# Kernel optimization log

Measured on AMD Instinct MI355X. Metric: run time of the kernel, lower is better.

Reference implementation:

```python
import jax, jax.numpy as jnp
import numpy as np

H1 = 51  # lstm1 hidden size
H3 = 1   # lstm3 hidden size


def _lstm_cell(x, h, c, W_ih, W_hh, b_ih, b_hh):
    # PyTorch LSTMCell: gates ordered (i, f, g, o)
    g = x @ W_ih.T + b_ih + h @ W_hh.T + b_hh
    i, f, gg, o = jnp.split(g, 4, axis=-1)
    c2 = jax.nn.sigmoid(f) * c + jax.nn.sigmoid(i) * jnp.tanh(gg)
    h2 = jax.nn.sigmoid(o) * jnp.tanh(c2)
    return h2, c2


def setup_inputs() -> dict:
    key = jax.random.key(0)
    ks = jax.random.split(key, 9)
    B, T = 2048, 2000
    s1 = 1.0 / np.sqrt(H1)
    s3 = 1.0 / np.sqrt(H3)
    u = lambda k, shape, s: jax.random.uniform(k, shape, jnp.float32, -s, s)
    return {
        "input": jax.random.normal(ks[0], (B, T), jnp.float32),
        "W_ih1": u(ks[1], (4 * H1, 1), s1),
        "W_hh1": u(ks[2], (4 * H1, H1), s1),
        "b_ih1": u(ks[3], (4 * H1,), s1),
        "b_hh1": u(ks[4], (4 * H1,), s1),
        "W_ih3": u(ks[5], (4 * H3, H1), s3),
        "W_hh3": u(ks[6], (4 * H3, H3), s3),
        "b_ih3": u(ks[7], (4 * H3,), s3),
        "b_hh3": u(ks[8], (4 * H3,), s3),
        "future": 0,
    }


def reference(input, W_ih1, W_hh1, b_ih1, b_hh1, W_ih3, W_hh3, b_ih3, b_hh3, future):
    B, T = input.shape
    dt = input.dtype
    h1 = jnp.zeros((B, H1), dt)
    c1 = jnp.zeros((B, H1), dt)
    h3 = jnp.zeros((B, H3), dt)
    c3 = jnp.zeros((B, H3), dt)

    def step(carry, x_t):
        h1, c1, h3, c3 = carry
        h1, c1 = _lstm_cell(x_t, h1, c1, W_ih1, W_hh1, b_ih1, b_hh1)
        # NOTE: original feeds c_t (cell state) into lstm3 and emits c_t3
        h3, c3 = _lstm_cell(c1, h3, c3, W_ih3, W_hh3, b_ih3, b_hh3)
        return (h1, c1, h3, c3), c3

    xs = input.T[:, :, None]  # [T, B, 1]
    carry, outs = jax.lax.scan(step, (h1, c1, h3, c3), xs)

    if future > 0:
        def fstep(carry, _):
            h1, c1, h3, c3 = carry
            h1, c1 = _lstm_cell(c3, h1, c1, W_ih1, W_hh1, b_ih1, b_hh1)
            h3, c3 = _lstm_cell(c1, h3, c3, W_ih3, W_hh3, b_ih3, b_hh3)
            return (h1, c1, h3, c3), c3

        carry, fouts = jax.lax.scan(fstep, carry, None, length=future)
        outs = jnp.concatenate([outs, fouts], axis=0)

    # [T(+future), B, 1] -> [B, T(+future)]
    return outs[:, :, 0].T
```

## Files before the change

kernel.cpp:

```cpp
#include <hip/hip_runtime.h>
#include <hip/hip_bf16.h>

#define SEQT 2000
#define NB   2048
#define H1   51
#define MROW 16
#define NBLK (NB / MROW)
#define PADK 168
#define OSTR 65

#define L2E  1.4426950408889634f
#define L2E2 2.8853900817779268f

typedef float f32x4 __attribute__((ext_vector_type(4)));
typedef short s16x8 __attribute__((ext_vector_type(8)));
typedef unsigned u32x4 __attribute__((ext_vector_type(4)));
typedef unsigned u32x2 __attribute__((ext_vector_type(2)));

#if __has_builtin(__builtin_amdgcn_exp2f)
#define EXP2F(x) __builtin_amdgcn_exp2f(x)
#else
#define EXP2F(x) __expf((x) * 0.6931471805599453f)
#endif

template <bool B> struct BoolC { static constexpr bool value = B; };

__device__ __forceinline__ short f2bf(float f) { __hip_bfloat16 b(f); return *(short*)&b; }
__device__ __forceinline__ float bf2f(short s) { __hip_bfloat16 b; *(short*)&b = s; return (float)b; }
__device__ __forceinline__ float rbf(float f) { return bf2f(f2bf(f)); }
__device__ __forceinline__ float fastrcp(float x) { return __builtin_amdgcn_rcpf(x); }
__device__ __forceinline__ float tanhfast(float x) {
    return 1.f - 2.f * fastrcp(EXP2F(x * L2E2) + 1.f);
}

__device__ __forceinline__ unsigned rne_bf16(float v) {
    unsigned b = __float_as_uint(v);
    return (b + 0x7fffu + ((b >> 16) & 1u)) >> 16;
}
__device__ __forceinline__ unsigned pack_hilo(float v) {
    const unsigned hh = rne_bf16(v);
    const float hi = __uint_as_float(hh << 16);
    const unsigned hl = rne_bf16(v - hi);
    return hh | (hl << 16);
}

__device__ __forceinline__ f32x4 mfma16(s16x8 a, s16x8 b, f32x4 c) {
    return __builtin_amdgcn_mfma_f32_16x16x32_bf16(a, b, c, 0, 0, 0);
}


__device__ __forceinline__ float aval(const float* __restrict__ W_hh1,
                                      const float* __restrict__ W_ih1,
                                      const float* __restrict__ b_ih1,
                                      const float* __restrict__ b_hh1,
                                      int n, float sc, bool vr, int k) {
    if (!vr) return 0.f;
    if (k < 96) {
        const int gp = k >> 3, j = k & 7;
        const int u = 4 * ((gp >> 2) * 4 + (j >> 1)) + (gp & 3);
        return rbf(sc * W_hh1[n * H1 + u]);
    } else if (k < 102) {
        const int u = 48 + ((k - 96) >> 1);
        return rbf(sc * W_hh1[n * H1 + u]);
    } else if (k < 104) {
        return rbf(sc * W_ih1[n]);
    } else if (k < 152) {
        const int d = k - 104;
        const int gp = d >> 2;
        const int u = 4 * ((gp >> 2) * 4 + (d & 3)) + (gp & 3);
        const float wv = sc * W_hh1[n * H1 + u];
        return wv - rbf(wv);
    } else if (k < 155) {
        const int u = 48 + (k - 152);
        const float wv = sc * W_hh1[n * H1 + u];
        return wv - rbf(wv);
    } else if (k == 155) {
        const float wv = sc * W_ih1[n];
        return wv - rbf(wv);
    } else if (k == 156) {
        return rbf(sc * (b_ih1[n] + b_hh1[n]));
    } else if (k == 157) {
        const float bv = sc * (b_ih1[n] + b_hh1[n]);
        return bv - rbf(bv);
    }
    return 0.f;
}

template <int SL, int NTc>
__device__ __forceinline__ void run_tiles(const s16x8 (&Wfr)[4][5], const s16x8 (&hf)[5],
                                          float (&c1st)[4], short* __restrict__ Hw,
                                          float* __restrict__ C1w,
                                          const int iloc, const int kq) {
    f32x4 acc[4];
#pragma unroll
    for (int i = 0; i < NTc; ++i) {
        f32x4 a = (f32x4){0.f, 0.f, 0.f, 0.f};
        a = mfma16(Wfr[i][0], hf[0], a);
        a = mfma16(Wfr[i][1], hf[1], a);
        a = mfma16(Wfr[i][2], hf[2], a);
        a = mfma16(Wfr[i][3], hf[3], a);
        a = mfma16(Wfr[i][4], hf[4], a);
        acc[i] = a;
    }
    unsigned hp[4];
    float cl[4];
#pragma unroll
    for (int i = 0; i < NTc; ++i) {
        const float ei = EXP2F(acc[i][0]);
        const float ef = EXP2F(acc[i][1]);
        const float eg = EXP2F(acc[i][2]);
        const float eo = EXP2F(acc[i][3]);
        const float pf = 1.f + ef, pi_ = 1.f + ei, pg = 1.f + eg, mg = 1.f - eg;
        const float pp = pi_ * pg;
        float c1 = c1st[i];
        c1 = fmaf(c1, pp, pf * mg) * fastrcp(pf * pp);
        c1st[i] = c1;
        cl[i] = c1;
        const float ec = EXP2F(fminf(115.4f, c1 * -L2E2));
        const float h1 = (1.f - ec) * fastrcp((1.f + eo) * (1.f + ec));
        const __hip_bfloat16 bh(h1);
        const float df = h1 - (float)bh;
        const __hip_bfloat16 bl(df);
        hp[i] = (unsigned)*(const unsigned short*)&bh |
                ((unsigned)*(const unsigned short*)&bl << 16);
    }
    const int base = iloc * PADK;
    if (NTc == 4) {
        *(u32x4*)&Hw[base + (SL * 4 + kq) * 8] =
            (u32x4){hp[0], hp[1], hp[2], hp[3]};
        const unsigned s01 = (hp[0] & 0xffffu) | (hp[1] << 16);
        const unsigned s23 = (hp[2] & 0xffffu) | (hp[3] << 16);
        *(u32x2*)&Hw[base + 104 + (SL * 4 + kq) * 4] = (u32x2){s01, s23};
        *(f32x4*)&C1w[iloc * 52 + SL * 16 + kq * 4] =
            (f32x4){cl[0], cl[1], cl[2], cl[3]};
    } else {
        const bool ok = (48 + kq) < H1;
        *(unsigned*)&Hw[base + (ok ? 96 + 2 * kq : 160)] = hp[0];
        Hw[base + (ok ? 152 + kq : 164)] = (short)hp[0];
        C1w[iloc * 52 + 48 + kq] = cl[0];
    }
}

__device__ __forceinline__ void xchunk_fill(const float* __restrict__ input, int r0, int c,
                                            int lane, unsigned (*Xb)[64 * 16]) {
    const int m = lane & 15, q = lane >> 4;
    const int tt = c * 64 + q * 16;
    f32x4 v[4];
    if (tt < SEQT) {
        const float* src = input + (size_t)(r0 + m) * SEQT + tt;
#pragma unroll
        for (int p = 0; p < 4; ++p) v[p] = *(const f32x4*)(src + 4 * p);
    } else {
#pragma unroll
        for (int p = 0; p < 4; ++p) v[p] = (f32x4){0.f, 0.f, 0.f, 0.f};
    }
#pragma unroll
    for (int p = 0; p < 4; ++p)
#pragma unroll
        for (int j = 0; j < 4; ++j)
            Xb[c & 1][(q * 16 + p * 4 + j) * 16 + m] = pack_hilo(v[p][j]);
}

__global__ void __launch_bounds__(256)
__attribute__((amdgpu_waves_per_eu(1)))
lstm_fused_kernel(const float* __restrict__ input,
                  const float* __restrict__ W_ih1,
                  const float* __restrict__ W_hh1,
                  const float* __restrict__ b_ih1,
                  const float* __restrict__ b_hh1,
                  const float* __restrict__ W_ih3,
                  const float* __restrict__ W_hh3,
                  const float* __restrict__ b_ih3,
                  const float* __restrict__ b_hh3,
                  float* __restrict__ out) {
    const int t = threadIdx.x;
    const int w = t >> 6;
    const int lane = t & 63;
    const int iloc = lane & 15, kq = lane >> 4;
    const int r0 = blockIdx.x * MROW;

    __shared__ short Hst[2][MROW * PADK];
    __shared__ float C1buf[2][MROW * 52];
    __shared__ float Obuf[2][MROW * OSTR];
    __shared__ unsigned Xbuf[2][64 * 16];

    const int NT = (w == 1) ? 1 : 4;
    const int tb = (w == 0) ? 0 : (w == 1) ? 12 : (w == 2) ? 4 : 8;

    s16x8 Wfr[4][5];
#pragma unroll
    for (int i = 0; i < 4; ++i) {
        if (i < NT) {
            const int np = (tb + i) * 16 + iloc;
            const int u_r = np >> 2, g_r = np & 3;
            const int n = g_r * H1 + u_r;
            const bool vr = (u_r < H1);
            const float sc = (g_r == 2) ? -L2E2 : -L2E;
#pragma unroll
            for (int kt = 0; kt < 5; ++kt) {
                s16x8 bf;
#pragma unroll
                for (int j = 0; j < 8; ++j)
                    bf[j] = f2bf(aval(W_hh1, W_ih1, b_ih1, b_hh1, n, sc, vr,
                                      kt * 32 + kq * 8 + j));
                Wfr[i][kt] = bf;
            }
        }
    }

    const int g3 = lane >> 4;
    const float scg3 = (g3 == 2) ? L2E2 : -L2E;
    float Wz[52];
    if (w == 1) {
#pragma unroll
        for (int p = 0; p < 52; ++p) {
            const int u = (p < 48) ? (16 * (p >> 4) + 4 * (p & 3) + ((p >> 2) & 3))
                                   : p;
            Wz[p] = (u < H1) ? scg3 * W_ih3[g3 * H1 + u] : 0.f;
        }
    }
    const float whh3g = scg3 * W_hh3[g3];
    const float b3g = scg3 * (b_ih3[g3] + b_hh3[g3]);
    const float ag = (g3 == 2) ? -2.f : 1.f;
    const float bg = (g3 == 2) ? 1.f : 0.f;

    for (int idx = t; idx < 2 * MROW * PADK; idx += 256)
        ((short*)Hst)[idx] = 0;
    for (int idx = t; idx < 2 * MROW * 52; idx += 256)
        ((float*)C1buf)[idx] = 0.f;
    __syncthreads();
    if (t < MROW) {
        const int m = t;
#pragma unroll
        for (int p = 0; p < 2; ++p) {
            Hst[p][m * PADK + 156] = (short)0x3F80;
            Hst[p][m * PADK + 157] = (short)0x3F80;
        }
        const float x0 = input[(size_t)(r0 + m) * SEQT];
        const unsigned xp = pack_hilo(x0);
        Hst[1][m * PADK + 102] = (short)xp;
        Hst[1][m * PADK + 103] = (short)(xp >> 16);
        Hst[1][m * PADK + 155] = (short)xp;
    }
    if (w == 1) {
        xchunk_fill(input, r0, 0, lane, Xbuf);
        xchunk_fill(input, r0, 1, lane, Xbuf);
    }
    float c1st[4] = {0.f, 0.f, 0.f, 0.f};
    float h3 = 0.f, c3 = 0.f;
    float h3b = 0.f;

    auto lstm3_step = [&](const f32x4 (&c1v)[13], int s) {
        float d0a = 0.f, d1a = 0.f, d2a = 0.f, d3a = 0.f;
        float d0b = 0.f, d1b = 0.f, d2b = 0.f, d3b = 0.f;
#pragma unroll
        for (int j = 0; j < 13; ++j) {
            if ((j & 1) == 0) {
                d0a = fmaf(Wz[4 * j + 0], c1v[j][0], d0a);
                d1a = fmaf(Wz[4 * j + 1], c1v[j][1], d1a);
                d2a = fmaf(Wz[4 * j + 2], c1v[j][2], d2a);
                d3a = fmaf(Wz[4 * j + 3], c1v[j][3], d3a);
            } else {
                d0b = fmaf(Wz[4 * j + 0], c1v[j][0], d0b);
                d1b = fmaf(Wz[4 * j + 1], c1v[j][1], d1b);
                d2b = fmaf(Wz[4 * j + 2], c1v[j][2], d2b);
                d3b = fmaf(Wz[4 * j + 3], c1v[j][3], d3b);
            }
        }
        const float z = ((d0a + d0b) + (d1a + d1b)) +
                        ((d2a + d2b) + (d3a + d3b));
        const float pre = z + fmaf(whh3g, h3b, b3g);
        const float act = bg + ag * fastrcp(EXP2F(pre) + 1.f);
        const float act1 = __shfl_xor(act, 16, 64);
        const float act2 = __shfl_xor(act, 32, 64);
        const float act3 = __shfl_xor(act, 48, 64);
        if (lane < MROW) {
            c3 = act1 * c3 + act * act2;
            h3 = act3 * tanhfast(c3);
            Obuf[(s >> 6) & 1][lane * OSTR + (s & 63)] = c3;
        }
        h3b = __shfl(h3, lane & 15, 64);
    };

    auto do_pair = [&](const int tsE, auto fillc, auto dumpc) {
        constexpr bool FILL = decltype(fillc)::value;
        constexpr bool DUMP = decltype(dumpc)::value;
        unsigned pv2 = 0;
        __syncthreads();
        {
            s16x8 hf[5];
#pragma unroll
            for (int kt = 0; kt < 5; ++kt)
                hf[kt] = *(const s16x8*)&Hst[1][iloc * PADK + kt * 32 + kq * 8];
            f32x4 c1v[13];
            unsigned pv1 = 0;
            if (w == 1) {
                const float* cr = &C1buf[1][(lane & 15) * 52];
#pragma unroll
                for (int j = 0; j < 13; ++j)
                    c1v[j] = *(const f32x4*)(cr + 4 * j);
                const int t1 = tsE + 1;
                pv1 = Xbuf[(t1 >> 6) & 1][(t1 & 63) * 16 + (lane & 15)];
                if (tsE + 2 < SEQT) {
                    const int t2 = tsE + 2;
                    pv2 = Xbuf[(t2 >> 6) & 1][(t2 & 63) * 16 + (lane & 15)];
                }
            }
            f32x4 xv[4];
            if (FILL && w == 1) {
                const int fc = (tsE >> 6) + 1;
                const int fm = lane & 15, fq = lane >> 4;
                const int tt = fc * 64 + fq * 16;
                if (tt < SEQT) {
                    const float* src = input + (size_t)(r0 + fm) * SEQT + tt;
#pragma unroll
                    for (int p = 0; p < 4; ++p) xv[p] = *(const f32x4*)(src + 4 * p);
                } else {
#pragma unroll
                    for (int p = 0; p < 4; ++p) xv[p] = (f32x4){0.f, 0.f, 0.f, 0.f};
                }
            }
            short* Hw = &Hst[0][0];
            float* C1w = &C1buf[0][0];
            if (w == 0) {
                run_tiles<0, 4>(Wfr, hf, c1st, Hw, C1w, iloc, kq);
            } else if (w == 2) {
                run_tiles<1, 4>(Wfr, hf, c1st, Hw, C1w, iloc, kq);
            } else if (w == 3) {
                run_tiles<2, 4>(Wfr, hf, c1st, Hw, C1w, iloc, kq);
            } else {
                const int m2 = lane & 15;
                *(unsigned*)&Hw[m2 * PADK + 102] = pv1;
                Hw[m2 * PADK + 155] = (short)pv1;
                run_tiles<3, 1>(Wfr, hf, c1st, Hw, C1w, iloc, kq);
                if (tsE > 0)
                    lstm3_step(c1v, tsE - 1);
            }
            if (FILL && w == 1) {
                const int fc = (tsE >> 6) + 1;
                const int fm = lane & 15, fq = lane >> 4;
#pragma unroll
                for (int p = 0; p < 4; ++p)
#pragma unroll
                    for (int j = 0; j < 4; ++j)
                        Xbuf[fc & 1][(fq * 16 + p * 4 + j) * 16 + fm] =
                            pack_hilo(xv[p][j]);
            }
        }
        __syncthreads();
        {
            const int tsO = tsE + 1;
            s16x8 hf[5];
#pragma unroll
            for (int kt = 0; kt < 5; ++kt)
                hf[kt] = *(const s16x8*)&Hst[0][iloc * PADK + kt * 32 + kq * 8];
            f32x4 c1v[13];
            if (w == 1) {
                const float* cr = &C1buf[0][(lane & 15) * 52];
#pragma unroll
                for (int j = 0; j < 13; ++j)
                    c1v[j] = *(const f32x4*)(cr + 4 * j);
            }
            if (DUMP) {
                const int c = (tsO >> 6) - 1;
#pragma unroll
                for (int rep = 0; rep < 4; ++rep) {
                    const int row = w + 4 * rep;
                    out[(size_t)(r0 + row) * SEQT + c * 64 + lane] =
                        Obuf[c & 1][row * OSTR + lane];
                }
            }
            short* Hw = &Hst[1][0];
            float* C1w = &C1buf[1][0];
            if (w == 0) {
                run_tiles<0, 4>(Wfr, hf, c1st, Hw, C1w, iloc, kq);
            } else if (w == 2) {
                run_tiles<1, 4>(Wfr, hf, c1st, Hw, C1w, iloc, kq);
            } else if (w == 3) {
                run_tiles<2, 4>(Wfr, hf, c1st, Hw, C1w, iloc, kq);
            } else {
                if (tsE + 2 < SEQT) {
                    const int m2 = lane & 15;
                    *(unsigned*)&Hw[m2 * PADK + 102] = pv2;
                    Hw[m2 * PADK + 155] = (short)pv2;
                }
                run_tiles<3, 1>(Wfr, hf, c1st, Hw, C1w, iloc, kq);
                lstm3_step(c1v, tsO - 1);
            }
        }
    };

#pragma unroll 1
    for (int c = 0; c < 32; ++c) {
        const int base = c << 6;
        int p0 = 0;
        if (c >= 1 && c < 31) {
            do_pair(base, BoolC<true>{}, BoolC<true>{});
            p0 = 1;
        } else if (c == 31) {
            do_pair(base, BoolC<false>{}, BoolC<true>{});
            p0 = 1;
        }
        const int npairs = (c == 31) ? 8 : 32;
#pragma unroll 1
        for (int p = p0; p < npairs; ++p)
            do_pair(base + (p << 1), BoolC<false>{}, BoolC<false>{});
    }

    __syncthreads();
    if (w == 1) {
        f32x4 c1v[13];
        const float* cr = &C1buf[1][(lane & 15) * 52];
#pragma unroll
        for (int j = 0; j < 13; ++j)
            c1v[j] = *(const f32x4*)(cr + 4 * j);
        lstm3_step(c1v, SEQT - 1);
    }

    __syncthreads();
    {
        const int row = t >> 4, pos = t & 15;
        out[(size_t)(r0 + row) * SEQT + 1984 + pos] = Obuf[1][row * OSTR + pos];
    }
}

extern "C" void kernel_launch(void* const* d_in, const int* in_sizes, int n_in,
                              void* d_out, int out_size, void* d_ws, size_t ws_size,
                              hipStream_t stream) {
    const float* input = (const float*)d_in[0];
    const float* W_ih1 = (const float*)d_in[1];
    const float* W_hh1 = (const float*)d_in[2];
    const float* b_ih1 = (const float*)d_in[3];
    const float* b_hh1 = (const float*)d_in[4];
    const float* W_ih3 = (const float*)d_in[5];
    const float* W_hh3 = (const float*)d_in[6];
    const float* b_ih3 = (const float*)d_in[7];
    const float* b_hh3 = (const float*)d_in[8];
    float* out = (float*)d_out;

    lstm_fused_kernel<<<NBLK, 256, 0, stream>>>(
        input, W_ih1, W_hh1, b_ih1, b_hh1, W_ih3, W_hh3, b_ih3, b_hh3, out);
}
```

Measured before the change: 1.298 ms.

## Distribute lstm3 input projection across waves and specialize per-wave loops

Each wave now folds its own c1 values into partial lstm3 gate dot-products (4 gates) right after computing them, and writes 16 partial sums per row to shared memory. This replaces the 52-element c1 buffer and the serial 52-term dot product on wave 1. The pair loop is also templated on wave id, first and last step, so branches become compile-time and each wave gets its own specialized code path. The cost moves into more FMAs per wave and a larger unrolled code body, in exchange for a shorter critical path on wave 1.

```diff
diff --git a/kernel.cpp b/kernel.cpp
--- a/kernel.cpp
+++ b/kernel.cpp
@@ -24,6 +24,7 @@
 #endif
 
 template <bool B> struct BoolC { static constexpr bool value = B; };
+template <int V>  struct IntC  { static constexpr int  value = V; };
 
 __device__ __forceinline__ short f2bf(float f) { __hip_bfloat16 b(f); return *(short*)&b; }
 __device__ __forceinline__ float bf2f(short s) { __hip_bfloat16 b; *(short*)&b = s; return (float)b; }
@@ -88,8 +89,9 @@
 
 template <int SL, int NTc>
 __device__ __forceinline__ void run_tiles(const s16x8 (&Wfr)[4][5], const s16x8 (&hf)[5],
-                                          float (&c1st)[4], short* __restrict__ Hw,
-                                          float* __restrict__ C1w,
+                                          float (&c1st)[4], const float (&W3c)[4][4],
+                                          short* __restrict__ Hw,
+                                          float* __restrict__ Zw,
                                           const int iloc, const int kq) {
     f32x4 acc[4];
 #pragma unroll
@@ -103,7 +105,7 @@
         acc[i] = a;
     }
     unsigned hp[4];
-    float cl[4];
+    float zp0 = 0.f, zp1 = 0.f, zp2 = 0.f, zp3 = 0.f;
 #pragma unroll
     for (int i = 0; i < NTc; ++i) {
         const float ei = EXP2F(acc[i][0]);
@@ -115,7 +117,10 @@
         float c1 = c1st[i];
         c1 = fmaf(c1, pp, pf * mg) * fastrcp(pf * pp);
         c1st[i] = c1;
-        cl[i] = c1;
+        zp0 = fmaf(W3c[i][0], c1, zp0);
+        zp1 = fmaf(W3c[i][1], c1, zp1);
+        zp2 = fmaf(W3c[i][2], c1, zp2);
+        zp3 = fmaf(W3c[i][3], c1, zp3);
         const float ec = EXP2F(fminf(115.4f, c1 * -L2E2));
         const float h1 = (1.f - ec) * fastrcp((1.f + eo) * (1.f + ec));
         const __hip_bfloat16 bh(h1);
@@ -131,14 +136,12 @@
         const unsigned s01 = (hp[0] & 0xffffu) | (hp[1] << 16);
         const unsigned s23 = (hp[2] & 0xffffu) | (hp[3] << 16);
         *(u32x2*)&Hw[base + 104 + (SL * 4 + kq) * 4] = (u32x2){s01, s23};
-        *(f32x4*)&C1w[iloc * 52 + SL * 16 + kq * 4] =
-            (f32x4){cl[0], cl[1], cl[2], cl[3]};
     } else {
         const bool ok = (48 + kq) < H1;
         *(unsigned*)&Hw[base + (ok ? 96 + 2 * kq : 160)] = hp[0];
         Hw[base + (ok ? 152 + kq : 164)] = (short)hp[0];
-        C1w[iloc * 52 + 48 + kq] = cl[0];
-    }
+    }
+    *(f32x4*)Zw = (f32x4){zp0, zp1, zp2, zp3};
 }
 
 __device__ __forceinline__ void xchunk_fill(const float* __restrict__ input, int r0, int c,
@@ -180,9 +183,9 @@
     const int r0 = blockIdx.x * MROW;
 
     __shared__ short Hst[2][MROW * PADK];
-    __shared__ float C1buf[2][MROW * 52];
     __shared__ float Obuf[2][MROW * OSTR];
     __shared__ unsigned Xbuf[2][64 * 16];
+    __shared__ float Zbuf[2][16][16][4];
 
     const int NT = (w == 1) ? 1 : 4;
     const int tb = (w == 0) ? 0 : (w == 1) ? 12 : (w == 2) ? 4 : 8;
@@ -208,17 +211,18 @@
         }
     }
 
+    float W3c[4][4];
+#pragma unroll
+    for (int i = 0; i < 4; ++i) {
+        const int u = (tb + i) * 4 + kq;
+        const bool ok = (i < NT) && (u < H1);
+#pragma unroll
+        for (int g = 0; g < 4; ++g)
+            W3c[i][g] = ok ? ((g == 2) ? L2E2 : -L2E) * W_ih3[g * H1 + u] : 0.f;
+    }
+
     const int g3 = lane >> 4;
     const float scg3 = (g3 == 2) ? L2E2 : -L2E;
-    float Wz[52];
-    if (w == 1) {
-#pragma unroll
-        for (int p = 0; p < 52; ++p) {
-            const int u = (p < 48) ? (16 * (p >> 4) + 4 * (p & 3) + ((p >> 2) & 3))
-                                   : p;
-            Wz[p] = (u < H1) ? scg3 * W_ih3[g3 * H1 + u] : 0.f;
-        }
-    }
     const float whh3g = scg3 * W_hh3[g3];
     const float b3g = scg3 * (b_ih3[g3] + b_hh3[g3]);
     const float ag = (g3 == 2) ? -2.f : 1.f;
@@ -226,8 +230,6 @@
 
     for (int idx = t; idx < 2 * MROW * PADK; idx += 256)
         ((short*)Hst)[idx] = 0;
-    for (int idx = t; idx < 2 * MROW * 52; idx += 256)
-        ((float*)C1buf)[idx] = 0.f;
     __syncthreads();
     if (t < MROW) {
         const int m = t;
@@ -250,25 +252,12 @@
     float h3 = 0.f, c3 = 0.f;
     float h3b = 0.f;
 
-    auto lstm3_step = [&](const f32x4 (&c1v)[13], int s) {
-        float d0a = 0.f, d1a = 0.f, d2a = 0.f, d3a = 0.f;
-        float d0b = 0.f, d1b = 0.f, d2b = 0.f, d3b = 0.f;
-#pragma unroll
-        for (int j = 0; j < 13; ++j) {
-            if ((j & 1) == 0) {
-                d0a = fmaf(Wz[4 * j + 0], c1v[j][0], d0a);
-                d1a = fmaf(Wz[4 * j + 1], c1v[j][1], d1a);
-                d2a = fmaf(Wz[4 * j + 2], c1v[j][2], d2a);
-                d3a = fmaf(Wz[4 * j + 3], c1v[j][3], d3a);
-            } else {
-                d0b = fmaf(Wz[4 * j + 0], c1v[j][0], d0b);
-                d1b = fmaf(Wz[4 * j + 1], c1v[j][1], d1b);
-                d2b = fmaf(Wz[4 * j + 2], c1v[j][2], d2b);
-                d3b = fmaf(Wz[4 * j + 3], c1v[j][3], d3b);
-            }
-        }
-        const float z = ((d0a + d0b) + (d1a + d1b)) +
-                        ((d2a + d2b) + (d3a + d3b));
+    auto lstm3_step = [&](const float (&zv)[16], int s) {
+        const float z =
+            (((zv[0] + zv[1]) + (zv[2] + zv[3])) +
+             ((zv[4] + zv[5]) + (zv[6] + zv[7]))) +
+            (((zv[8] + zv[9]) + (zv[10] + zv[11])) +
+             ((zv[12] + zv[13]) + (zv[14] + zv[15])));
         const float pre = z + fmaf(whh3g, h3b, b3g);
         const float act = bg + ag * fastrcp(EXP2F(pre) + 1.f);
         const float act1 = __shfl_xor(act, 16, 64);
@@ -282,9 +271,14 @@
         h3b = __shfl(h3, lane & 15, 64);
     };
 
-    auto do_pair = [&](const int tsE, auto fillc, auto dumpc) {
-        constexpr bool FILL = decltype(fillc)::value;
-        constexpr bool DUMP = decltype(dumpc)::value;
+    auto do_pair = [&](auto wc, auto fc, auto dc, auto fic, auto lac,
+                       const int tsE) {
+        constexpr int W = decltype(wc)::value;
+        constexpr bool FILL = decltype(fc)::value;
+        constexpr bool DUMP = decltype(dc)::value;
+        constexpr bool FIRST = decltype(fic)::value;
+        constexpr bool LAST = decltype(lac)::value;
+        constexpr int SL = (W == 0) ? 0 : (W == 1) ? 3 : (W == 2) ? 1 : 2;
         unsigned pv2 = 0;
         __syncthreads();
         {
@@ -292,25 +286,26 @@
 #pragma unroll
             for (int kt = 0; kt < 5; ++kt)
                 hf[kt] = *(const s16x8*)&Hst[1][iloc * PADK + kt * 32 + kq * 8];
-            f32x4 c1v[13];
+            float zv[16];
             unsigned pv1 = 0;
-            if (w == 1) {
-                const float* cr = &C1buf[1][(lane & 15) * 52];
-#pragma unroll
-                for (int j = 0; j < 13; ++j)
-                    c1v[j] = *(const f32x4*)(cr + 4 * j);
+            if constexpr (W == 1) {
+                if constexpr (!FIRST) {
+#pragma unroll
+                    for (int q = 0; q < 16; ++q)
+                        zv[q] = Zbuf[1][q][lane & 15][g3];
+                }
                 const int t1 = tsE + 1;
                 pv1 = Xbuf[(t1 >> 6) & 1][(t1 & 63) * 16 + (lane & 15)];
-                if (tsE + 2 < SEQT) {
+                if constexpr (!LAST) {
                     const int t2 = tsE + 2;
                     pv2 = Xbuf[(t2 >> 6) & 1][(t2 & 63) * 16 + (lane & 15)];
                 }
             }
             f32x4 xv[4];
-            if (FILL && w == 1) {
-                const int fc = (tsE >> 6) + 1;
+            if constexpr (FILL && W == 1) {
+                const int fc2 = (tsE >> 6) + 1;
                 const int fm = lane & 15, fq = lane >> 4;
-                const int tt = fc * 64 + fq * 16;
+                const int tt = fc2 * 64 + fq * 16;
                 if (tt < SEQT) {
                     const float* src = input + (size_t)(r0 + fm) * SEQT + tt;
 #pragma unroll
@@ -321,29 +316,25 @@
                 }
             }
             short* Hw = &Hst[0][0];
-            float* C1w = &C1buf[0][0];
-            if (w == 0) {
-                run_tiles<0, 4>(Wfr, hf, c1st, Hw, C1w, iloc, kq);
-            } else if (w == 2) {
-                run_tiles<1, 4>(Wfr, hf, c1st, Hw, C1w, iloc, kq);
-            } else if (w == 3) {
-                run_tiles<2, 4>(Wfr, hf, c1st, Hw, C1w, iloc, kq);
-            } else {
+            float* Zw = &Zbuf[0][SL * 4 + kq][iloc][0];
+            if constexpr (W == 1) {
                 const int m2 = lane & 15;
                 *(unsigned*)&Hw[m2 * PADK + 102] = pv1;
                 Hw[m2 * PADK + 155] = (short)pv1;
-                run_tiles<3, 1>(Wfr, hf, c1st, Hw, C1w, iloc, kq);
-                if (tsE > 0)
-                    lstm3_step(c1v, tsE - 1);
-            }
-            if (FILL && w == 1) {
-                const int fc = (tsE >> 6) + 1;
+                run_tiles<3, 1>(Wfr, hf, c1st, W3c, Hw, Zw, iloc, kq);
+                if constexpr (!FIRST)
+                    lstm3_step(zv, tsE - 1);
+            } else {
+                run_tiles<SL, 4>(Wfr, hf, c1st, W3c, Hw, Zw, iloc, kq);
+            }
+            if constexpr (FILL && W == 1) {
+                const int fc2 = (tsE >> 6) + 1;
                 const int fm = lane & 15, fq = lane >> 4;
 #pragma unroll
                 for (int p = 0; p < 4; ++p)
 #pragma unroll
                     for (int j = 0; j < 4; ++j)
-                        Xbuf[fc & 1][(fq * 16 + p * 4 + j) * 16 + fm] =
+                        Xbuf[fc2 & 1][(fq * 16 + p * 4 + j) * 16 + fm] =
                             pack_hilo(xv[p][j]);
             }
         }
@@ -354,67 +345,70 @@
 #pragma unroll
             for (int kt = 0; kt < 5; ++kt)
                 hf[kt] = *(const s16x8*)&Hst[0][iloc * PADK + kt * 32 + kq * 8];
-            f32x4 c1v[13];
-            if (w == 1) {
-                const float* cr = &C1buf[0][(lane & 15) * 52];
-#pragma unroll
-                for (int j = 0; j < 13; ++j)
-                    c1v[j] = *(const f32x4*)(cr + 4 * j);
-            }
-            if (DUMP) {
+            float zv[16];
+            if constexpr (W == 1) {
+#pragma unroll
+                for (int q = 0; q < 16; ++q)
+                    zv[q] = Zbuf[0][q][lane & 15][g3];
+            }
+            if constexpr (DUMP) {
                 const int c = (tsO >> 6) - 1;
 #pragma unroll
                 for (int rep = 0; rep < 4; ++rep) {
-                    const int row = w + 4 * rep;
+                    const int row = W + 4 * rep;
                     out[(size_t)(r0 + row) * SEQT + c * 64 + lane] =
                         Obuf[c & 1][row * OSTR + lane];
                 }
             }
             short* Hw = &Hst[1][0];
-            float* C1w = &C1buf[1][0];
-            if (w == 0) {
-                run_tiles<0, 4>(Wfr, hf, c1st, Hw, C1w, iloc, kq);
-            } else if (w == 2) {
-                run_tiles<1, 4>(Wfr, hf, c1st, Hw, C1w, iloc, kq);
-            } else if (w == 3) {
-                run_tiles<2, 4>(Wfr, hf, c1st, Hw, C1w, iloc, kq);
-            } else {
-                if (tsE + 2 < SEQT) {
+            float* Zw = &Zbuf[1][SL * 4 + kq][iloc][0];
+            if constexpr (W == 1) {
+                if constexpr (!LAST) {
                     const int m2 = lane & 15;
                     *(unsigned*)&Hw[m2 * PADK + 102] = pv2;
                     Hw[m2 * PADK + 155] = (short)pv2;
                 }
-                run_tiles<3, 1>(Wfr, hf, c1st, Hw, C1w, iloc, kq);
-                lstm3_step(c1v, tsO - 1);
+                run_tiles<3, 1>(Wfr, hf, c1st, W3c, Hw, Zw, iloc, kq);
+                lstm3_step(zv, tsO - 1);
+            } else {
+                run_tiles<SL, 4>(Wfr, hf, c1st, W3c, Hw, Zw, iloc, kq);
             }
         }
     };
 
+    auto run_chunks = [&](auto wc) {
+        constexpr BoolC<false> F{};
+        constexpr BoolC<true>  T{};
+        do_pair(wc, F, F, T, F, 0);
 #pragma unroll 1
-    for (int c = 0; c < 32; ++c) {
-        const int base = c << 6;
-        int p0 = 0;
-        if (c >= 1 && c < 31) {
-            do_pair(base, BoolC<true>{}, BoolC<true>{});
-            p0 = 1;
-        } else if (c == 31) {
-            do_pair(base, BoolC<false>{}, BoolC<true>{});
-            p0 = 1;
-        }
-        const int npairs = (c == 31) ? 8 : 32;
+        for (int p = 1; p < 32; ++p)
+            do_pair(wc, F, F, F, F, p << 1);
 #pragma unroll 1
-        for (int p = p0; p < npairs; ++p)
-            do_pair(base + (p << 1), BoolC<false>{}, BoolC<false>{});
-    }
+        for (int c = 1; c < 31; ++c) {
+            do_pair(wc, T, T, F, F, c << 6);
+#pragma unroll 1
+            for (int p = 1; p < 32; ++p)
+                do_pair(wc, F, F, F, F, (c << 6) + (p << 1));
+        }
+        do_pair(wc, F, T, F, F, 31 << 6);
+#pragma unroll 1
+        for (int p = 1; p < 7; ++p)
+            do_pair(wc, F, F, F, F, (31 << 6) + (p << 1));
+        do_pair(wc, F, F, F, T, (31 << 6) + 14);
+    };
+
+    if (w == 0)      run_chunks(IntC<0>{});
+    else if (w == 1) run_chunks(IntC<1>{});
+    else if (w == 2) run_chunks(IntC<2>{});
+    else             run_chunks(IntC<3>{});
 
     __syncthreads();
     if (w == 1) {
-        f32x4 c1v[13];
-        const float* cr = &C1buf[1][(lane & 15) * 52];
-#pragma unroll
-        for (int j = 0; j < 13; ++j)
-            c1v[j] = *(const f32x4*)(cr + 4 * j);
-        lstm3_step(c1v, SEQT - 1);
+        float zv[16];
+#pragma unroll
+        for (int q = 0; q < 16; ++q)
+            zv[q] = Zbuf[1][q][lane & 15][g3];
+        lstm3_step(zv, SEQT - 1);
     }
 
     __syncthreads();
```

Measured after the change: 1.167 ms. 10.1% less time.
